# Performance work log

Measured on AMD Instinct MI355X. Metric: run time of the kernel, lower is better.

Reference implementation:

```python
import jax, jax.numpy as jnp
import numpy as np

N = 10000   # num_nodes (= input feature dim, identity-style features)
E = 320000  # edges (avg degree 32)
P = 200000  # candidate node pairs
H1, H2 = 32, 16


def gcn_conv(x, W, b, edge_index, num_nodes):
    # PyG GCNConv: add self-loops, symmetric D^-1/2 (A+I) D^-1/2 normalization,
    # linear transform, scatter-add aggregation, then bias.
    loop = jnp.arange(num_nodes)
    src = jnp.concatenate([edge_index[0], loop])
    dst = jnp.concatenate([edge_index[1], loop])
    deg = jax.ops.segment_sum(jnp.ones_like(src, dtype=x.dtype), dst,
                              num_segments=num_nodes)  # includes self-loop, so deg >= 1
    dinv = jax.lax.rsqrt(deg)
    norm = dinv[src] * dinv[dst]                       # [E+N]
    h = x @ W                                          # [N, out]
    out = jax.ops.segment_sum(h[src] * norm[:, None], dst, num_segments=num_nodes)
    return out + b


def setup_inputs() -> dict:
    key = jax.random.key(0)
    ks = jax.random.split(key, 9)
    x = jax.random.normal(ks[0], (N, N), dtype=jnp.float32)
    edge_index = jax.random.randint(ks[1], (2, E), 0, N)
    pair_index = jax.random.randint(ks[2], (P, 2), 0, N)
    W1 = jax.random.normal(ks[3], (N, H1), dtype=jnp.float32) * 0.01
    b1 = jnp.zeros((H1,), jnp.float32)
    W2 = jax.random.normal(ks[4], (H1, H2), dtype=jnp.float32) * 0.1
    b2 = jnp.zeros((H2,), jnp.float32)
    Wfc = jax.random.normal(ks[5], (2 * H2, 1), dtype=jnp.float32) * 0.1
    bfc = jnp.zeros((1,), jnp.float32)
    return {"x": x, "edge_index": edge_index, "pair_index": pair_index,
            "W1": W1, "b1": b1, "W2": W2, "b2": b2, "Wfc": Wfc, "bfc": bfc}


def reference(x, edge_index, pair_index, W1, b1, W2, b2, Wfc, bfc):
    h = jax.nn.relu(gcn_conv(x, W1, b1, edge_index, N))   # [N, 32]
    h = gcn_conv(h, W2, b2, edge_index, N)                # [N, 16]
    pair = jnp.concatenate([h[pair_index[:, 0]], h[pair_index[:, 1]]], axis=1)  # [P, 32]
    return jax.nn.sigmoid(pair @ Wfc + bfc)               # [P, 1]
```

## Files before the change

### kernel.cpp

```cpp
#include <hip/hip_runtime.h>
#include <math.h>

#define NN 10000
#define EE 320000
#define PP 200000
#define NTILES 320
#define KSPL 512
#define NSPL 20

typedef _Float16 h8v __attribute__((ext_vector_type(8)));
typedef __attribute__((ext_vector_type(4))) float f4v;

#define GLOAD_LDS16(gsrc, ldst)                                                        \
    __builtin_amdgcn_global_load_lds((const __attribute__((address_space(1))) void*)(gsrc), \
                                     (__attribute__((address_space(3))) void*)(ldst), 16, 0, 0)

__device__ __forceinline__ ushort f2h(float f) {
    union { _Float16 h; ushort u; } c;
    c.h = (_Float16)f;
    return c.u;
}

__global__ void k_deg_count(const int* __restrict__ dst, int* __restrict__ degi) {
    int e = blockIdx.x * blockDim.x + threadIdx.x;
    if (e < EE) atomicAdd(&degi[dst[e]], 1);
}

__global__ void k_dinv(const int* __restrict__ degi, float* __restrict__ dinv) {
    int n = blockIdx.x * blockDim.x + threadIdx.x;
    if (n < NN) dinv[n] = rsqrtf((float)(degi[n] + 1));
}

__global__ void k_wprep(const float* __restrict__ W1, ushort* __restrict__ wf) {
    int t = blockIdx.x * blockDim.x + threadIdx.x;
    if (t >= NTILES * 2 * 64 * 8) return;
    int e = t & 7, lane = (t >> 3) & 63, ct = (t >> 9) & 1, g = t >> 10;
    int col = ct * 16 + (lane & 15);
    int k = g * 32 + (lane >> 4) * 8 + e;
    wf[t] = (k < NN) ? f2h(W1[(long)k * 32 + col]) : (ushort)0;
}

__global__ __launch_bounds__(64) void k_gemm1(const float* __restrict__ x,
                                              const ushort* __restrict__ w1f,
                                              const float* __restrict__ zp,
                                              float* __restrict__ h1_part) {
    __shared__ __align__(16) float xs[16][260];
    const int lane = threadIdx.x;
    const int fl = lane & 15;
    const int khi = lane >> 4;
    const int ks = blockIdx.y;
    const int wrow0 = blockIdx.x * 16;
    const long NN2 = (long)NN * NN;

    f4v acc0 = (f4v){0.f, 0.f, 0.f, 0.f};
    f4v acc1 = (f4v){0.f, 0.f, 0.f, 0.f};

#pragma unroll
    for (int half = 0; half < 2; ++half) {
        const int kbase = ks * KSPL + half * 256;
        const int gbase8 = ks * 16 + half * 8;

#pragma unroll
        for (int j = 0; j < 16; ++j) {
            long flat = (long)(wrow0 + j) * NN + kbase + lane * 4;
            const float* src = (flat + 4 <= NN2) ? (x + flat) : zp;
            GLOAD_LDS16(src, &xs[j][0]);
        }
        h8v wr[8][2];
#pragma unroll
        for (int kk = 0; kk < 8; ++kk)
#pragma unroll
            for (int ct = 0; ct < 2; ++ct)
                wr[kk][ct] = *(const h8v*)(w1f + ((long)((gbase8 + kk) * 2 + ct) * 64 + lane) * 8);

        asm volatile("s_waitcnt vmcnt(0)" ::: "memory");
        __builtin_amdgcn_sched_barrier(0);

#pragma unroll
        for (int kk = 0; kk < 8; ++kk) {
            const float4* ap = (const float4*)&xs[fl][kk * 32 + khi * 8];
            float4 f0 = ap[0];
            float4 f1 = ap[1];
            union { h8v v; _Float16 h[8]; } a;
            a.h[0] = (_Float16)f0.x; a.h[1] = (_Float16)f0.y;
            a.h[2] = (_Float16)f0.z; a.h[3] = (_Float16)f0.w;
            a.h[4] = (_Float16)f1.x; a.h[5] = (_Float16)f1.y;
            a.h[6] = (_Float16)f1.z; a.h[7] = (_Float16)f1.w;
            acc0 = __builtin_amdgcn_mfma_f32_16x16x32_f16(a.v, wr[kk][0], acc0, 0, 0, 0);
            acc1 = __builtin_amdgcn_mfma_f32_16x16x32_f16(a.v, wr[kk][1], acc1, 0, 0, 0);
        }
        asm volatile("s_waitcnt lgkmcnt(0)" ::: "memory");
        __builtin_amdgcn_sched_barrier(0);
    }

    const long pbase = (long)ks * NN * 32;
#pragma unroll
    for (int ct = 0; ct < 2; ++ct) {
        f4v a = ct ? acc1 : acc0;
        const int col = ct * 16 + fl;
#pragma unroll
        for (int r = 0; r < 4; ++r) {
            int g = wrow0 + khi * 4 + r;
            h1_part[pbase + (long)g * 32 + col] = a[r];
        }
    }
}

__global__ void k_selfinit1(const float4* __restrict__ h1_part4, const float* __restrict__ dinv,
                            float4* __restrict__ h1_pre4, float4* __restrict__ out14) {
    int t = blockIdx.x * blockDim.x + threadIdx.x;
    if (t >= NN * 8) return;
    float4 s = make_float4(0.f, 0.f, 0.f, 0.f);
#pragma unroll
    for (int ks = 0; ks < NSPL; ++ks) {
        float4 v = h1_part4[(long)ks * NN * 8 + t];
        s.x += v.x; s.y += v.y; s.z += v.z; s.w += v.w;
    }
    int n = t >> 3;
    float d2 = dinv[n] * dinv[n];
    h1_pre4[t] = s;
    out14[t] = make_float4(s.x * d2, s.y * d2, s.z * d2, s.w * d2);
}

__global__ void k_scatter1(const int* __restrict__ src, const int* __restrict__ dst,
                           const float* __restrict__ dinv, const float* __restrict__ h1_pre,
                           float* __restrict__ out1) {
    int t = blockIdx.x * blockDim.x + threadIdx.x;
    if (t >= EE * 32) return;
    int e = t >> 5, c = t & 31;
    int s = src[e], d = dst[e];
    float nrm = dinv[s] * dinv[d];
    atomicAdd(&out1[d * 32 + c], h1_pre[s * 32 + c] * nrm);
}

__global__ __launch_bounds__(256) void k_gemm2(const float* __restrict__ out1,
                                               const float* __restrict__ W2,
                                               const float* __restrict__ b1,
                                               const float* __restrict__ dinv,
                                               float* __restrict__ h2_pre,
                                               float* __restrict__ out2) {
    __shared__ float w2s[512];
    __shared__ float b1s[32];
    int tid = threadIdx.x;
    w2s[tid] = W2[tid & 511];
    if (tid < 256) w2s[256 + tid] = W2[256 + tid];
    if (tid < 32) b1s[tid] = b1[tid];
    __syncthreads();
    int c = tid & 15, yloc = tid >> 4;
    int n = blockIdx.x * 16 + yloc;
    if (n < NN) {
        float a = 0.f;
#pragma unroll
        for (int k = 0; k < 32; ++k) {
            float v = fmaxf(out1[n * 32 + k] + b1s[k], 0.f);
            a += v * w2s[k * 16 + c];
        }
        h2_pre[n * 16 + c] = a;
        float di = dinv[n];
        out2[n * 16 + c] = di * di * a;
    }
}

__global__ void k_scatter2(const int* __restrict__ src, const int* __restrict__ dst,
                           const float* __restrict__ dinv, const float* __restrict__ h2_pre,
                           float* __restrict__ out2) {
    int t = blockIdx.x * blockDim.x + threadIdx.x;
    if (t >= EE * 16) return;
    int e = t >> 4, c = t & 15;
    int s = src[e], d = dst[e];
    float nrm = dinv[s] * dinv[d];
    atomicAdd(&out2[d * 16 + c], h2_pre[s * 16 + c] * nrm);
}

__global__ void k_final2(const float* __restrict__ out2, const float* __restrict__ b2,
                         const float* __restrict__ Wfc, float* __restrict__ s_arr,
                         float* __restrict__ t_arr) {
    int n = blockIdx.x * blockDim.x + threadIdx.x;
    if (n >= NN) return;
    float s = 0.f, t = 0.f;
#pragma unroll
    for (int c = 0; c < 16; ++c) {
        float v = out2[n * 16 + c] + b2[c];
        s += v * Wfc[c];
        t += v * Wfc[16 + c];
    }
    s_arr[n] = s;
    t_arr[n] = t;
}

__global__ void k_pairs(const int* __restrict__ pair, const float* __restrict__ s_arr,
                        const float* __restrict__ t_arr, const float* __restrict__ bfc,
                        float* __restrict__ out) {
    int p = blockIdx.x * blockDim.x + threadIdx.x;
    if (p >= PP) return;
    const int2 ab = ((const int2*)pair)[p];
    float z = s_arr[ab.x] + t_arr[ab.y] + bfc[0];
    out[p] = 1.f / (1.f + expf(-z));
}

extern "C" void kernel_launch(void* const* d_in, const int* in_sizes, int n_in,
                              void* d_out, int out_size, void* d_ws, size_t ws_size,
                              hipStream_t stream) {
    const float* x    = (const float*)d_in[0];
    const int*   edge = (const int*)d_in[1];
    const int*   pair = (const int*)d_in[2];
    const float* W1   = (const float*)d_in[3];
    const float* b1   = (const float*)d_in[4];
    const float* W2   = (const float*)d_in[5];
    const float* b2   = (const float*)d_in[6];
    const float* Wfc  = (const float*)d_in[7];
    const float* bfc  = (const float*)d_in[8];
    float* out = (float*)d_out;
    float* ws  = (float*)d_ws;

    const int* src = edge;
    const int* dst = edge + EE;

    int*    degi    = (int*)ws;
    float*  dinv    = ws + NN;
    float*  h1_pre  = ws + 2 * NN;
    float*  out1    = ws + 34 * NN;
    float*  h2_pre  = ws + 66 * NN;
    float*  out2    = ws + 82 * NN;
    float*  s_arr   = ws + 98 * NN;
    float*  t_arr   = ws + 99 * NN;
    float*  zp      = ws + 100 * NN;
    ushort* w1f     = (ushort*)(ws + 100 * NN + 256);
    float*  h1_part = ws + 100 * NN + 256 + 163840;

    hipMemsetAsync(degi, 0, NN * sizeof(int), stream);
    hipMemsetAsync(zp, 0, 1024, stream);

    k_deg_count<<<(EE + 255) / 256, 256, 0, stream>>>(dst, degi);
    k_dinv<<<(NN + 255) / 256, 256, 0, stream>>>(degi, dinv);
    k_wprep<<<(NTILES * 2 * 64 * 8 + 255) / 256, 256, 0, stream>>>(W1, w1f);

    k_gemm1<<<dim3(625, NSPL), 64, 0, stream>>>(x, w1f, zp, h1_part);

    k_selfinit1<<<(NN * 8 + 255) / 256, 256, 0, stream>>>(
        (const float4*)h1_part, dinv, (float4*)h1_pre, (float4*)out1);
    k_scatter1<<<(EE * 32 + 255) / 256, 256, 0, stream>>>(src, dst, dinv, h1_pre, out1);

    k_gemm2<<<(NN + 15) / 16, 256, 0, stream>>>(out1, W2, b1, dinv, h2_pre, out2);

    k_scatter2<<<(EE * 16 + 255) / 256, 256, 0, stream>>>(src, dst, dinv, h2_pre, out2);

    k_final2<<<(NN + 255) / 256, 256, 0, stream>>>(out2, b2, Wfc, s_arr, t_arr);
    k_pairs<<<(PP + 255) / 256, 256, 0, stream>>>(pair, s_arr, t_arr, bfc, out);
}
```

Measured before the change: 195.0 us.

## Project layer-2 features onto FC weights before aggregation to scatter scalars

Because the second GCN aggregation and the final linear layer are both linear, the 16-wide node features are projected onto the two halves of Wfc first, giving two scalars per node. The edge scatter then does two scalar atomics per edge instead of sixteen, and the separate final-reduction kernel is removed, with the bias terms folded into the self-loop init. This cuts atomic traffic and a launch, at the cost of a different floating-point summation order.

```diff
diff --git a/kernel.cpp b/kernel.cpp
--- a/kernel.cpp
+++ b/kernel.cpp
@@ -133,59 +133,62 @@
     atomicAdd(&out1[d * 32 + c], h1_pre[s * 32 + c] * nrm);
 }
 
-__global__ __launch_bounds__(256) void k_gemm2(const float* __restrict__ out1,
-                                               const float* __restrict__ W2,
-                                               const float* __restrict__ b1,
-                                               const float* __restrict__ dinv,
-                                               float* __restrict__ h2_pre,
-                                               float* __restrict__ out2) {
+__global__ __launch_bounds__(256) void k_gemm2p(const float* __restrict__ out1,
+                                                const float* __restrict__ W2,
+                                                const float* __restrict__ b1,
+                                                const float* __restrict__ b2,
+                                                const float* __restrict__ Wfc,
+                                                const float* __restrict__ dinv,
+                                                float* __restrict__ u_arr,
+                                                float* __restrict__ v_arr,
+                                                float* __restrict__ s_arr,
+                                                float* __restrict__ t_arr) {
     __shared__ float w2s[512];
     __shared__ float b1s[32];
+    __shared__ float wfs[32];
     int tid = threadIdx.x;
     w2s[tid] = W2[tid & 511];
     if (tid < 256) w2s[256 + tid] = W2[256 + tid];
-    if (tid < 32) b1s[tid] = b1[tid];
+    if (tid < 32) { b1s[tid] = b1[tid]; wfs[tid] = Wfc[tid]; }
     __syncthreads();
     int c = tid & 15, yloc = tid >> 4;
     int n = blockIdx.x * 16 + yloc;
-    if (n < NN) {
-        float a = 0.f;
-#pragma unroll
-        for (int k = 0; k < 32; ++k) {
-            float v = fmaxf(out1[n * 32 + k] + b1s[k], 0.f);
-            a += v * w2s[k * 16 + c];
-        }
-        h2_pre[n * 16 + c] = a;
-        float di = dinv[n];
-        out2[n * 16 + c] = di * di * a;
-    }
-}
-
-__global__ void k_scatter2(const int* __restrict__ src, const int* __restrict__ dst,
-                           const float* __restrict__ dinv, const float* __restrict__ h2_pre,
-                           float* __restrict__ out2) {
-    int t = blockIdx.x * blockDim.x + threadIdx.x;
-    if (t >= EE * 16) return;
-    int e = t >> 4, c = t & 15;
+    if (n >= NN) return;
+    float a = 0.f;
+#pragma unroll
+    for (int k = 0; k < 32; ++k) {
+        float vv = fmaxf(out1[n * 32 + k] + b1s[k], 0.f);
+        a += vv * w2s[k * 16 + c];
+    }
+    float sp = a * wfs[c];
+    float tp = a * wfs[16 + c];
+#pragma unroll
+    for (int d = 8; d >= 1; d >>= 1) {
+        sp += __shfl_xor(sp, d);
+        tp += __shfl_xor(tp, d);
+    }
+    if (c == 0) {
+        float S0 = 0.f, T0 = 0.f;
+#pragma unroll
+        for (int k = 0; k < 16; ++k) { S0 += b2[k] * wfs[k]; T0 += b2[k] * wfs[16 + k]; }
+        float d2 = dinv[n] * dinv[n];
+        u_arr[n] = sp;
+        v_arr[n] = tp;
+        s_arr[n] = d2 * sp + S0;
+        t_arr[n] = d2 * tp + T0;
+    }
+}
+
+__global__ void k_scatter2p(const int* __restrict__ src, const int* __restrict__ dst,
+                            const float* __restrict__ dinv, const float* __restrict__ u_arr,
+                            const float* __restrict__ v_arr, float* __restrict__ s_arr,
+                            float* __restrict__ t_arr) {
+    int e = blockIdx.x * blockDim.x + threadIdx.x;
+    if (e >= EE) return;
     int s = src[e], d = dst[e];
     float nrm = dinv[s] * dinv[d];
-    atomicAdd(&out2[d * 16 + c], h2_pre[s * 16 + c] * nrm);
-}
-
-__global__ void k_final2(const float* __restrict__ out2, const float* __restrict__ b2,
-                         const float* __restrict__ Wfc, float* __restrict__ s_arr,
-                         float* __restrict__ t_arr) {
-    int n = blockIdx.x * blockDim.x + threadIdx.x;
-    if (n >= NN) return;
-    float s = 0.f, t = 0.f;
-#pragma unroll
-    for (int c = 0; c < 16; ++c) {
-        float v = out2[n * 16 + c] + b2[c];
-        s += v * Wfc[c];
-        t += v * Wfc[16 + c];
-    }
-    s_arr[n] = s;
-    t_arr[n] = t;
+    atomicAdd(&s_arr[d], nrm * u_arr[s]);
+    atomicAdd(&t_arr[d], nrm * v_arr[s]);
 }
 
 __global__ void k_pairs(const int* __restrict__ pair, const float* __restrict__ s_arr,
@@ -220,8 +223,8 @@
     float*  dinv    = ws + NN;
     float*  h1_pre  = ws + 2 * NN;
     float*  out1    = ws + 34 * NN;
-    float*  h2_pre  = ws + 66 * NN;
-    float*  out2    = ws + 82 * NN;
+    float*  u_arr   = ws + 66 * NN;
+    float*  v_arr   = ws + 67 * NN;
     float*  s_arr   = ws + 98 * NN;
     float*  t_arr   = ws + 99 * NN;
     float*  zp      = ws + 100 * NN;
@@ -239,12 +242,14 @@
 
     k_selfinit1<<<(NN * 8 + 255) / 256, 256, 0, stream>>>(
         (const float4*)h1_part, dinv, (float4*)h1_pre, (float4*)out1);
+
     k_scatter1<<<(EE * 32 + 255) / 256, 256, 0, stream>>>(src, dst, dinv, h1_pre, out1);
 
-    k_gemm2<<<(NN + 15) / 16, 256, 0, stream>>>(out1, W2, b1, dinv, h2_pre, out2);
-
-    k_scatter2<<<(EE * 16 + 255) / 256, 256, 0, stream>>>(src, dst, dinv, h2_pre, out2);
-
-    k_final2<<<(NN + 255) / 256, 256, 0, stream>>>(out2, b2, Wfc, s_arr, t_arr);
+    k_gemm2p<<<(NN + 15) / 16, 256, 0, stream>>>(out1, W2, b1, b2, Wfc, dinv,
+                                                 u_arr, v_arr, s_arr, t_arr);
+
+    k_scatter2p<<<(EE + 255) / 256, 256, 0, stream>>>(src, dst, dinv, u_arr, v_arr,
+                                                      s_arr, t_arr);
+
     k_pairs<<<(PP + 255) / 256, 256, 0, stream>>>(pair, s_arr, t_arr, bfc, out);
 }
```

After: 215.4 us. 10.5% more time.
